# Optimization experiments

Measured on AMD Instinct MI355X. Metric: run time of the kernel, lower is better.

The kernel has to match this reference:

```python
import jax, jax.numpy as jnp
import numpy as np

WS = 8
SHIFT = 4


def _cpb_constants(ws):
    rc = np.arange(-(ws - 1), ws, dtype=np.float32)
    gh, gw = np.meshgrid(rc, rc, indexing='ij')
    table = np.stack([gh, gw], axis=-1)[None]  # (1, 2ws-1, 2ws-1, 2)
    table = table / (ws - 1) * 8.0
    table = np.sign(table) * np.log2(np.abs(table) + 1.0) / np.log2(8.0)
    c = np.arange(ws)
    ch, cw = np.meshgrid(c, c, indexing='ij')
    flat = np.stack([ch.ravel(), cw.ravel()])  # (2, N)
    rel = (flat[:, :, None] - flat[:, None, :]).transpose(1, 2, 0).copy()
    rel[..., 0] += ws - 1
    rel[..., 1] += ws - 1
    rel[..., 0] *= 2 * ws - 1
    rpi = rel.sum(-1)  # (N, N) int
    return table.astype(np.float32), rpi


def _attn_mask(H, W, ws, s):
    # Faithful to source: middle slice is slice(-ws, +s) (empty for H>ws+s)
    img = np.zeros((H, W), np.float32)
    cnt = 0
    for hs in (slice(0, -ws), slice(-ws, s), slice(-s, None)):
        for wsl in (slice(0, -ws), slice(-ws, s), slice(-s, None)):
            img[hs, wsl] = cnt
            cnt += 1
    mw = img.reshape(H // ws, ws, W // ws, ws).transpose(0, 2, 1, 3).reshape(-1, ws * ws)
    am = mw[:, None, :] - mw[:, :, None]
    return np.where(am != 0, -100.0, 0.0).astype(np.float32)


def _dwconv(x, w):
    return jax.lax.conv_general_dilated(
        x, w, (1, 1), 'SAME',
        dimension_numbers=('NCHW', 'OIHW', 'NCHW'),
        feature_group_count=x.shape[1])


def _ln_nchw(x, g, b, eps=8e-8):
    m = x.mean(1, keepdims=True)
    v = jnp.square(x - m).mean(1, keepdims=True)
    return (x - m) / jnp.sqrt(v + eps) * g[None, :, None, None] + b[None, :, None, None]


def setup_inputs() -> dict:
    key = jax.random.key(0)
    ks = jax.random.split(key, 16)
    B, C, H, W = 16, 512, 64, 64
    nh = 16
    hid = 4 * C
    w = lambda k, s: (jax.random.normal(k, s, dtype=jnp.float32) * 0.02)
    return {
        'x': jax.random.normal(ks[0], (B, C, H, W), dtype=jnp.float32),
        'lpu_w': w(ks[1], (C, 1, 3, 3)),
        'qkv_w': w(ks[2], (3 * C, C)),
        'out_w': w(ks[3], (C, C)),
        'cpb_w1': w(ks[4], (512, 2)),
        'cpb_w2': w(ks[5], (nh, 512)),
        'logits_scale': jnp.full((nh, 1, 1), np.log(10.0), dtype=jnp.float32),
        'gamma1': jnp.ones((C,), jnp.float32),
        'beta1': jnp.zeros((C,), jnp.float32),
        'gamma2': jnp.ones((C,), jnp.float32),
        'beta2': jnp.zeros((C,), jnp.float32),
        'pw1_w': w(ks[6], (hid, C)),
        'dw_w': w(ks[7], (hid, 1, 3, 3)),
        'pw2_w': w(ks[8], (C, hid)),
        'sr_scale': jnp.ones((), jnp.float32),
        'sr_bias': jnp.zeros((), jnp.float32),
        'rs1': jnp.ones((C,), jnp.float32),
        'rs2': jnp.ones((C,), jnp.float32),
    }


def reference(x, lpu_w, qkv_w, out_w, cpb_w1, cpb_w2, logits_scale,
              gamma1, beta1, gamma2, beta2, pw1_w, dw_w, pw2_w,
              sr_scale, sr_bias, rs1, rs2):
    B, C, H, W = x.shape
    ws, s = WS, SHIFT
    nh = logits_scale.shape[0]
    hd = C // nh
    N = ws * ws
    table_np, rpi = _cpb_constants(ws)
    table = jnp.asarray(table_np)
    mask = jnp.asarray(_attn_mask(H, W, ws, s))  # (nW, N, N)

    # LPU: x + depthwise conv
    x = x + _dwconv(x, lpu_w)
    x_temp = x

    # flatten to (B, HW, C); faithful roll over dims (1,2) = tokens AND channels
    x = x.reshape(B, C, H * W).transpose(0, 2, 1)
    x = jnp.roll(x, (-s, -s), axis=(1, 2))
    # window partition
    x = x.reshape(B, H // ws, ws, W // ws, ws, C).transpose(0, 1, 3, 2, 4, 5).reshape(-1, N, C)
    Bw = x.shape[0]

    qkv = (x @ qkv_w.T).reshape(Bw, N, 3, nh, hd).transpose(2, 0, 3, 1, 4)
    q, k, v = qkv[0], qkv[1], qkv[2]
    qn = q / jnp.maximum(jnp.linalg.norm(q, axis=-1, keepdims=True), 1e-12)
    kn = k / jnp.maximum(jnp.linalg.norm(k, axis=-1, keepdims=True), 1e-12)
    scale = jnp.exp(jnp.minimum(logits_scale, jnp.log(jnp.float32(100.0))))
    attn = jnp.einsum('bhid,bhjd->bhij', qn, kn) * scale[None]

    # continuous position bias
    tbl = jax.nn.hard_swish(table @ cpb_w1.T) @ cpb_w2.T  # (1, 2ws-1, 2ws-1, nh)
    tbl = tbl.reshape(-1, nh)
    bias = tbl[rpi.reshape(-1)].reshape(N, N, nh).transpose(2, 0, 1)
    bias = 16.0 * jax.nn.sigmoid(bias)
    attn = attn + bias[None]

    nW = mask.shape[0]
    attn = (attn.reshape(Bw // nW, nW, nh, N, N) + mask[None, :, None]).reshape(-1, nh, N, N)
    # faithful: nn.Softmax(1) -> softmax over HEAD axis
    attn = jax.nn.softmax(attn, axis=1)

    o = jnp.einsum('bhij,bhjd->bhid', attn, v).transpose(0, 2, 1, 3).reshape(Bw, N, C)
    o = o @ out_w.T

    o = o.reshape(B, H // ws, ws, W // ws, ws, C)
    o = jnp.roll(o, (s, s), axis=(1, 2))  # faithful: rolls window-grid / row dims
    # faithful buggy un-partition: transpose(1,2) then reshape
    o = o.transpose(0, 2, 1, 3, 4, 5).reshape(B, C, H, W)

    x = rs1[None, :, None, None] * x_temp + _ln_nchw(o, gamma1, beta1)

    h = jnp.einsum('bchw,oc->bohw', x, pw1_w)
    h = h + _dwconv(h, dw_w)
    h = sr_scale * jnp.square(jax.nn.relu(h)) + sr_bias  # StarReLU
    y = jnp.einsum('bchw,oc->bohw', h, pw2_w)
    return rs2[None, :, None, None] * x + _ln_nchw(y, gamma2, beta2)
```

## Files before the change

kernel.cpp:

```cpp
#include <hip/hip_runtime.h>
#include <hip/hip_bf16.h>
#include <stdint.h>


typedef float f32x4 __attribute__((ext_vector_type(4)));
typedef short s16x8 __attribute__((ext_vector_type(8)));

__device__ __forceinline__ float b2f(short u) {
  return __uint_as_float(((unsigned)(unsigned short)u) << 16);
}
__device__ __forceinline__ short f2b(float f) {
  __hip_bfloat16 h = __float2bfloat16(f);
  short s;
  __builtin_memcpy(&s, &h, 2);
  return s;
}
__device__ __forceinline__ void gload16(const void* g, void* l) {
  __builtin_amdgcn_global_load_lds((const unsigned int*)g, (unsigned int*)l, 16, 0, 0);
}

__global__ __launch_bounds__(256) void k_f2b4(const float* __restrict__ s0, short* __restrict__ d0,
                                              const float* __restrict__ s1, short* __restrict__ d1,
                                              const float* __restrict__ s2, short* __restrict__ d2,
                                              const float* __restrict__ s3, short* __restrict__ d3) {
  int b = blockIdx.x;
  const float* s;
  short* d;
  int base;
  if (b < 768) { s = s0; d = d0; base = b * 1024; }
  else if (b < 1024) { s = s1; d = d1; base = (b - 768) * 1024; }
  else if (b < 2048) { s = s2; d = d2; base = (b - 1024) * 1024; }
  else { s = s3; d = d3; base = (b - 2048) * 1024; }
  int i = base + threadIdx.x * 4;
  f32x4 v = *(const f32x4*)&s[i];
  ushort4 o;
  o.x = (unsigned short)f2b(v[0]);
  o.y = (unsigned short)f2b(v[1]);
  o.z = (unsigned short)f2b(v[2]);
  o.w = (unsigned short)f2b(v[3]);
  *(ushort4*)&d[i] = o;
}

__global__ __launch_bounds__(64) void k_cpb(const float* __restrict__ w1,
                                            const float* __restrict__ w2,
                                            float* __restrict__ btab) {
  const int r = blockIdx.x;
  const int lane = threadIdx.x;
  const int ri = r / 15, rj = r % 15;
  float th = (float)(ri - 7) * (8.f / 7.f);
  float tw = (float)(rj - 7) * (8.f / 7.f);
  float gh = copysignf(log2f(fabsf(th) + 1.f) * (1.f / 3.f), th);
  float gw = copysignf(log2f(fabsf(tw) + 1.f) * (1.f / 3.f), tw);
  const int h = lane >> 2, pp = lane & 3;
  float acc = 0.f;
  for (int k = 0; k < 128; ++k) {
    int hh = pp * 128 + k;
    float a = gh * w1[hh * 2] + gw * w1[hh * 2 + 1];
    float r6 = fminf(fmaxf(a + 3.f, 0.f), 6.f);
    float hsw = a * r6 * (1.f / 6.f);
    acc += hsw * w2[h * 512 + hh];
  }
  acc += __shfl_xor(acc, 1);
  acc += __shfl_xor(acc, 2);
  if ((lane & 3) == 0) btab[h * 225 + r] = 16.f / (1.f + __expf(-acc));
}

__global__ __launch_bounds__(256) void k_lpu(const float* __restrict__ x,
                                             const float* __restrict__ lw,
                                             short* __restrict__ xt) {
  __shared__ float img[64 * 68];
  const int bc = blockIdx.x;
  const int c = bc & 511;
  const float* img_g = x + (size_t)bc * 4096;
  short* outp = xt + (size_t)bc * 4096;
  const int tid = threadIdx.x;
#pragma unroll
  for (int t = 0; t < 4; ++t) {
    int idx = t * 256 + tid;
    int h = idx >> 4, w4 = (idx & 15) * 4;
    f32x4 v = *(const f32x4*)&img_g[h * 64 + w4];
    *(f32x4*)&img[h * 68 + w4] = v;
  }
  float wreg[9];
#pragma unroll
  for (int t = 0; t < 9; ++t) wreg[t] = lw[c * 9 + t];
  __syncthreads();
  const int hb = tid >> 4, w0 = (tid & 15) * 4;
#pragma unroll
  for (int g = 0; g < 4; ++g) {
    int h = hb + g * 16;
    float row[3][6];
#pragma unroll
    for (int dr = 0; dr < 3; ++dr) {
      int hh = h - 1 + dr;
      if (hh < 0 || hh > 63) {
#pragma unroll
        for (int j = 0; j < 6; ++j) row[dr][j] = 0.f;
      } else {
        f32x4 m = *(const f32x4*)&img[hh * 68 + w0];
        row[dr][1] = m[0]; row[dr][2] = m[1]; row[dr][3] = m[2]; row[dr][4] = m[3];
        row[dr][0] = (w0 > 0) ? img[hh * 68 + w0 - 1] : 0.f;
        row[dr][5] = (w0 < 60) ? img[hh * 68 + w0 + 4] : 0.f;
      }
    }
    ushort4 o;
    unsigned short op[4];
#pragma unroll
    for (int p = 0; p < 4; ++p) {
      float acc = row[1][p + 1];
#pragma unroll
      for (int dr = 0; dr < 3; ++dr)
#pragma unroll
        for (int dc = 0; dc < 3; ++dc)
          acc += wreg[dr * 3 + dc] * row[dr][p + dc];
      op[p] = (unsigned short)f2b(acc);
    }
    o.x = op[0]; o.y = op[1]; o.z = op[2]; o.w = op[3];
    *(ushort4*)&outp[h * 64 + w0] = o;
  }
}

__global__ __launch_bounds__(256) void k_xpose(const short* __restrict__ xt,
                                               short* __restrict__ xw) {
  __shared__ short tile[64][132];
  const int tid = threadIdx.x;
  const int cq = blockIdx.x & 3;
  const int h = (blockIdx.x >> 2) & 63;
  const int b = blockIdx.x >> 8;
  const int c0 = cq * 128;
  for (int idx = tid; idx < 64 * 128; idx += 256) {
    int ww = idx & 63, cc = idx >> 6;
    int csrc = (c0 + cc + 4) & 511;
    tile[ww][cc] = xt[(((size_t)b * 512 + csrc) * 64 + h) * 64 + ww];
  }
  __syncthreads();
  for (int qd = tid; qd < 64 * 32; qd += 256) {
    int ws_ = qd >> 5, cqq = qd & 31, cc = cqq * 4;
    int t = (h * 64 + ws_ + 4092) & 4095;
    int hd = t >> 6, wd = t & 63;
    int tok = (b * 64 + (hd >> 3) * 8 + (wd >> 3)) * 64 + (hd & 7) * 8 + (wd & 7);
    ushort4 u = *(const ushort4*)&tile[ws_][cc];
    *(ushort4*)&xw[(size_t)tok * 512 + c0 + cc] = u;
  }
}

template <int EPI>
__global__ __launch_bounds__(256) void k_gemm(const short* __restrict__ A,
                                              const short* __restrict__ B,
                                              short* __restrict__ C,
                                              short* __restrict__ o4,
                                              const float* __restrict__ lsc,
                                              int N, int K, int gx) {
  __shared__ short smem[2 * 128 * 64];
  short* As = smem;
  short* Bs = smem + 128 * 64;
  const int nwg = gridDim.x;
  const int orig = blockIdx.x;
  const int wgid = (orig & 7) * (nwg >> 3) + (orig >> 3);
  const int bx = wgid % gx, by = wgid / gx;
  const int tid = threadIdx.x;
  const int lane = tid & 63, wid = tid >> 6;
  const int wm = wid >> 1, wn = wid & 1;
  const int m0 = by * 128, n0 = bx * 128;
  const f32x4 fz = {0.f, 0.f, 0.f, 0.f};
  f32x4 acc[4][4];
#pragma unroll
  for (int m = 0; m < 4; ++m)
#pragma unroll
    for (int n = 0; n < 4; ++n) acc[m][n] = fz;
  const int rst = lane >> 3;
  const int cst = ((lane & 7) ^ rst) * 8;
  const int l15 = lane & 15, l4 = lane >> 4, l7 = lane & 7;
  const short* ap[4];
  const short* bp[4];
#pragma unroll
  for (int i = 0; i < 4; ++i) {
    int r = (i * 4 + wid) * 8 + rst;
    ap[i] = A + (size_t)(m0 + r) * K + cst;
    bp[i] = B + (size_t)(n0 + r) * K + cst;
  }
  for (int k0 = 0; k0 < K; k0 += 64) {
#pragma unroll
    for (int i = 0; i < 4; ++i) {
      int rb = i * 4 + wid;
      gload16(ap[i], As + rb * 512);
      gload16(bp[i], Bs + rb * 512);
      ap[i] += 64;
      bp[i] += 64;
    }
    __syncthreads();
#pragma unroll
    for (int ks = 0; ks < 2; ++ks) {
      s16x8 af[4], bfr[4];
#pragma unroll
      for (int m = 0; m < 4; ++m) {
        int row = wm * 64 + m * 16 + l15;
        af[m] = *(const s16x8*)&As[row * 64 + (((ks * 4 + l4) ^ l7) * 8)];
      }
#pragma unroll
      for (int n = 0; n < 4; ++n) {
        int row = wn * 64 + n * 16 + l15;
        bfr[n] = *(const s16x8*)&Bs[row * 64 + (((ks * 4 + l4) ^ l7) * 8)];
      }
#pragma unroll
      for (int m = 0; m < 4; ++m)
#pragma unroll
        for (int n = 0; n < 4; ++n)
          acc[m][n] = __builtin_amdgcn_mfma_f32_16x16x32_bf16(af[m], bfr[n],
                                                              acc[m][n], 0, 0, 0);
    }
    __syncthreads();
  }
  if (EPI == 2 && n0 < 1024) {
    const int cb = n0 + wn * 64;
    if (cb < 1024) {
      const bool isq = cb < 512;
      float sc0 = 1.f, sc1 = 1.f;
      if (isq) {
        sc0 = __expf(fminf(lsc[cb >> 5], 4.605170185988092f));
        sc1 = __expf(fminf(lsc[(cb >> 5) + 1], 4.605170185988092f));
      }
#pragma unroll
      for (int m = 0; m < 4; ++m)
#pragma unroll
        for (int np = 0; np < 2; ++np)
#pragma unroll
          for (int r = 0; r < 4; ++r) {
            float s0 = acc[m][2 * np][r], s1 = acc[m][2 * np + 1][r];
            float ss = s0 * s0 + s1 * s1;
            ss += __shfl_xor(ss, 1);
            ss += __shfl_xor(ss, 2);
            ss += __shfl_xor(ss, 4);
            ss += __shfl_xor(ss, 8);
            float mul = (np ? sc1 : sc0) / fmaxf(sqrtf(ss), 1e-12f);
            acc[m][2 * np][r] = s0 * mul;
            acc[m][2 * np + 1][r] = s1 * mul;
          }
    }
  }
  short* ct = smem;
  const int colslot = tid & 15;
#pragma unroll
  for (int p = 0; p < 2; ++p) {
    if (p) __syncthreads();
#pragma unroll
    for (int mm = 0; mm < 2; ++mm) {
      int m = p * 2 + mm;
#pragma unroll
      for (int n = 0; n < 4; ++n)
#pragma unroll
        for (int r = 0; r < 4; ++r) {
          int lrow = wm * 32 + mm * 16 + l4 * 4 + r;
          int lc = wn * 64 + n * 16 + l15;
          ct[lrow * 136 + lc] = f2b(acc[m][n][r]);
        }
    }
    __syncthreads();
#pragma unroll
    for (int ps = 0; ps < 4; ++ps) {
      int lr = (tid >> 4) + ps * 16;
      s16x8 v = *(const s16x8*)&ct[lr * 136 + colslot * 8];
      int grow = m0 + (lr >> 5) * 64 + p * 32 + (lr & 31);
      int gcol = n0 + colslot * 8;
      if (EPI != 1) {
        *(s16x8*)&C[(size_t)grow * N + gcol] = v;
      } else {
        int win = grow >> 6, nn = grow & 63;
        int b = win >> 6, whs = (win >> 3) & 7, wws = win & 7;
        int ih = nn >> 3, iw = nn & 7;
        int wh = (whs + 4) & 7, ww = (wws + 4) & 7;
        int cp = ww * 64 + wh * 8 + ih;
        int hp = iw * 8 + (gcol >> 6);
        int wp = gcol & 63;
        *(s16x8*)&o4[(((size_t)b * 512 + cp) * 64 + hp) * 64 + wp] = v;
      }
    }
  }
}

__global__ __launch_bounds__(256) void k_attn(const short* __restrict__ qkv,
                                              const float* __restrict__ btab_g,
                                              short* __restrict__ o_ws) {
  __shared__ float btab[3600];
  __shared__ short vts[2][2048];
  __shared__ short pts[4][1024];
  const int tid = threadIdx.x, lane = tid & 63, wid = tid >> 6;
  const int win = blockIdx.x;
  const int l15 = lane & 15, l4 = lane >> 4;
  const int qrow0 = wid * 16;
  for (int i = tid; i < 3600; i += 256) btab[i] = btab_g[i];
  int baddr[4][4];
#pragma unroll
  for (int n = 0; n < 4; ++n)
#pragma unroll
    for (int r = 0; r < 4; ++r) {
      int i_ = qrow0 + l4 * 4 + r, j_ = n * 16 + l15;
      int dih = (i_ >> 3) - (j_ >> 3) + 7;
      int diw = (i_ & 7) - (j_ & 7) + 7;
      baddr[n][r] = dih * 15 + diw;
    }
  __syncthreads();
  const short* base = qkv + (size_t)win * 64 * 1536;
  const f32x4 fz = {0.f, 0.f, 0.f, 0.f};
  f32x4 sump[4] = {fz, fz, fz, fz};
#pragma unroll 2
  for (int h = 0; h < 16; ++h) {
    s16x8 qf = *(const s16x8*)(base + (size_t)(qrow0 + l15) * 1536 + h * 32 + l4 * 8);
#pragma unroll
    for (int n = 0; n < 4; ++n) {
      s16x8 kf = *(const s16x8*)(base + (size_t)(n * 16 + l15) * 1536 + 512 + h * 32 + l4 * 8);
      f32x4 s = __builtin_amdgcn_mfma_f32_16x16x32_bf16(qf, kf, fz, 0, 0, 0);
#pragma unroll
      for (int r = 0; r < 4; ++r)
        sump[n][r] += __expf(s[r] + btab[h * 225 + baddr[n][r]]);
    }
  }
  f32x4 rden[4];
#pragma unroll
  for (int n = 0; n < 4; ++n)
#pragma unroll
    for (int r = 0; r < 4; ++r) rden[n][r] = 1.f / sump[n][r];
  char* pt = (char*)pts[wid];
  {
    int j = tid & 63, d0 = (tid >> 6) * 8;
    s16x8 vv = *(const s16x8*)(base + (size_t)j * 1536 + 1024 + d0);
#pragma unroll
    for (int jj = 0; jj < 8; ++jj) {
      int d = d0 + jj;
      *(short*)((char*)vts[0] + ((d * 128 + j * 2) ^ ((d & 7) << 4))) = vv[jj];
    }
  }
  __syncthreads();
  for (int h = 0; h < 16; ++h) {
    const char* vcur = (const char*)vts[h & 1];
    if (h < 15) {
      int j = tid & 63, d0 = (tid >> 6) * 8;
      s16x8 vv = *(const s16x8*)(base + (size_t)j * 1536 + 1024 + (h + 1) * 32 + d0);
      char* vnxt = (char*)vts[(h + 1) & 1];
#pragma unroll
      for (int jj = 0; jj < 8; ++jj) {
        int d = d0 + jj;
        *(short*)(vnxt + ((d * 128 + j * 2) ^ ((d & 7) << 4))) = vv[jj];
      }
    }
    s16x8 qf = *(const s16x8*)(base + (size_t)(qrow0 + l15) * 1536 + h * 32 + l4 * 8);
#pragma unroll
    for (int n = 0; n < 4; ++n) {
      s16x8 kf = *(const s16x8*)(base + (size_t)(n * 16 + l15) * 1536 + 512 + h * 32 + l4 * 8);
      f32x4 s = __builtin_amdgcn_mfma_f32_16x16x32_bf16(qf, kf, fz, 0, 0, 0);
#pragma unroll
      for (int r = 0; r < 4; ++r) {
        float pv = __expf(s[r] + btab[h * 225 + baddr[n][r]]) * rden[n][r];
        int i_loc = l4 * 4 + r, j_ = n * 16 + l15;
        *(short*)(pt + ((i_loc * 128 + j_ * 2) ^ ((i_loc & 7) << 4))) = f2b(pv);
      }
    }
    f32x4 oacc[2] = {fz, fz};
#pragma unroll
    for (int kb = 0; kb < 2; ++kb) {
      s16x8 af = *(const s16x8*)(pt + ((l15 * 128 + kb * 64 + l4 * 16) ^ ((l15 & 7) << 4)));
#pragma unroll
      for (int db = 0; db < 2; ++db) {
        int d = db * 16 + l15;
        s16x8 bf = *(const s16x8*)(vcur + ((d * 128 + kb * 64 + l4 * 16) ^ ((d & 7) << 4)));
        oacc[db] = __builtin_amdgcn_mfma_f32_16x16x32_bf16(af, bf, oacc[db], 0, 0, 0);
      }
    }
    short* ob = o_ws + ((size_t)win * 64 + qrow0) * 512 + h * 32;
#pragma unroll
    for (int db = 0; db < 2; ++db)
#pragma unroll
      for (int r = 0; r < 4; ++r)
        ob[(size_t)(l4 * 4 + r) * 512 + db * 16 + l15] = f2b(oacc[db][r]);
    __syncthreads();
  }
}

__global__ __launch_bounds__(256) void k_ln1(const short* __restrict__ o4,
                                             const short* __restrict__ xt,
                                             const float* __restrict__ g1,
                                             const float* __restrict__ b1,
                                             const float* __restrict__ rs1,
                                             short* __restrict__ x2h) {
  __shared__ float reds[4][64], redq[4][64];
  __shared__ float mean_s[64], rstd_s[64];
  __shared__ short tile[128][66];
  const int tid = threadIdx.x;
  const int b = blockIdx.x >> 6, hp = blockIdx.x & 63;
  const int w = tid & 63, part = tid >> 6;
  const short* base = o4 + (size_t)b * 512 * 4096 + hp * 64;
  float s = 0.f, q = 0.f;
  for (int c = part; c < 512; c += 4) {
    float v = b2f(base[(size_t)c * 4096 + w]);
    s += v; q += v * v;
  }
  reds[part][w] = s; redq[part][w] = q;
  __syncthreads();
  if (tid < 64) {
    float S = 0.f, Q = 0.f;
    for (int i = 0; i < 4; ++i) { S += reds[i][tid]; Q += redq[i][tid]; }
    float m = S * (1.f / 512.f);
    float var = Q * (1.f / 512.f) - m * m;
    mean_s[tid] = m;
    rstd_s[tid] = rsqrtf(var + 8e-8f);
  }
  __syncthreads();
  const short* xtb = xt + (size_t)b * 512 * 4096 + hp * 64;
  for (int c0 = 0; c0 < 512; c0 += 128) {
    for (int cc = part; cc < 128; cc += 4) {
      int c = c0 + cc;
      float v = b2f(base[(size_t)c * 4096 + w]);
      float ln = (v - mean_s[w]) * rstd_s[w] * g1[c] + b1[c];
      float xv = rs1[c] * b2f(xtb[(size_t)c * 4096 + w]) + ln;
      tile[cc][w] = f2b(xv);
    }
    __syncthreads();
    short* xh = x2h + ((size_t)blockIdx.x * 64) * 512 + c0;
    for (int qd = tid; qd < 64 * 32; qd += 256) {
      int w_ = qd >> 5, cq = qd & 31, cc = cq * 4;
      ushort4 u;
      u.x = (unsigned short)tile[cc][w_];
      u.y = (unsigned short)tile[cc + 1][w_];
      u.z = (unsigned short)tile[cc + 2][w_];
      u.w = (unsigned short)tile[cc + 3][w_];
      *(ushort4*)&xh[(size_t)w_ * 512 + cc] = u;
    }
    __syncthreads();
  }
}

__global__ __launch_bounds__(256) void k_dwc2(const short* __restrict__ h1,
                                              const float* __restrict__ dw,
                                              const float* __restrict__ srs_p,
                                              const float* __restrict__ srb_p,
                                              short* __restrict__ h2) {
  __shared__ short tile[6 * 64 * 64];
  const int tid = threadIdx.x;
  const int cblk = blockIdx.x & 31;
  const int hq = (blockIdx.x >> 5) & 15;
  const int b = blockIdx.x >> 9;
  const int c0 = cblk * 64;
  const int h0 = hq * 4;
  for (int t = 0; t < 12; ++t) {
    int idx = t * 256 + tid;
    int cg = idx & 7;
    int wl = (idx >> 3) & 63;
    int rl = idx >> 9;
    int hr = h0 - 1 + rl;
    s16x8 v = {0, 0, 0, 0, 0, 0, 0, 0};
    if (hr >= 0 && hr < 64)
      v = *(const s16x8*)&h1[((size_t)b * 4096 + hr * 64 + wl) * 2048 + c0 + cg * 8];
    *(s16x8*)&tile[(rl * 64 + wl) * 64 + (cg ^ (wl & 7)) * 8] = v;
  }
  const int cg = tid & 7;
  const int wq = tid >> 3;
  float wt[9][8];
#pragma unroll
  for (int j = 0; j < 8; ++j) {
    int cch = c0 + cg * 8 + j;
#pragma unroll
    for (int t = 0; t < 9; ++t) wt[t][j] = dw[cch * 9 + t];
  }
  const float srs = *srs_p, srb = *srb_p;
  __syncthreads();
#pragma unroll
  for (int it = 0; it < 8; ++it) {
    int wl = wq + (it & 1) * 32;
    int rl = it >> 1;
    s16x8 ctr = *(const s16x8*)&tile[((rl + 1) * 64 + wl) * 64 + (cg ^ (wl & 7)) * 8];
    float acc[8];
#pragma unroll
    for (int j = 0; j < 8; ++j) acc[j] = b2f(ctr[j]);
#pragma unroll
    for (int dh = -1; dh <= 1; ++dh) {
      int row = rl + 1 + dh;
#pragma unroll
      for (int dwi = -1; dwi <= 1; ++dwi) {
        int wn = wl + dwi;
        if (wn < 0 || wn > 63) continue;
        s16x8 v = *(const s16x8*)&tile[(row * 64 + wn) * 64 + (cg ^ (wn & 7)) * 8];
        const float* wrow = wt[(dh + 1) * 3 + dwi + 1];
#pragma unroll
        for (int j = 0; j < 8; ++j) acc[j] += wrow[j] * b2f(v[j]);
      }
    }
    s16x8 o;
#pragma unroll
    for (int j = 0; j < 8; ++j) {
      float rr = fmaxf(acc[j], 0.f);
      o[j] = f2b(srs * rr * rr + srb);
    }
    *(s16x8*)&h2[((size_t)b * 4096 + (h0 + rl) * 64 + wl) * 2048 + c0 + cg * 8] = o;
  }
}

__global__ __launch_bounds__(256) void k_final(const short* __restrict__ y,
                                               const short* __restrict__ x2h,
                                               const float* __restrict__ g2,
                                               const float* __restrict__ b2p,
                                               const float* __restrict__ rs2,
                                               float* __restrict__ out) {
  __shared__ short yt[64][132];
  __shared__ short xt2[64][132];
  __shared__ float reds[4][64], redq[4][64];
  __shared__ float mean_s[64], rstd_s[64];
  const int tid = threadIdx.x;
  const int b = blockIdx.x >> 6, hh = blockIdx.x & 63;
  const int w = tid & 63, part = tid >> 6;
  const short* yb = y + (size_t)blockIdx.x * 64 * 512;
  const short* xb = x2h + (size_t)blockIdx.x * 64 * 512;
  float s = 0.f, q = 0.f;
  for (int c0 = 0; c0 < 512; c0 += 128) {
    for (int qd = tid; qd < 64 * 32; qd += 256) {
      int w_ = qd >> 5, g = qd & 31;
      *(ushort4*)&yt[w_][g * 4] = *(const ushort4*)&yb[(size_t)w_ * 512 + c0 + g * 4];
    }
    __syncthreads();
    for (int cc = part * 32; cc < part * 32 + 32; ++cc) {
      float v = b2f(yt[w][cc]);
      s += v; q += v * v;
    }
    __syncthreads();
  }
  reds[part][w] = s; redq[part][w] = q;
  __syncthreads();
  if (tid < 64) {
    float S = 0.f, Q = 0.f;
    for (int i = 0; i < 4; ++i) { S += reds[i][tid]; Q += redq[i][tid]; }
    float m = S * (1.f / 512.f);
    float var = Q * (1.f / 512.f) - m * m;
    mean_s[tid] = m;
    rstd_s[tid] = rsqrtf(var + 8e-8f);
  }
  __syncthreads();
  float* ob = out + (size_t)b * 512 * 4096 + hh * 64;
  for (int c0 = 0; c0 < 512; c0 += 128) {
    for (int qd = tid; qd < 64 * 32; qd += 256) {
      int w_ = qd >> 5, g = qd & 31;
      *(ushort4*)&yt[w_][g * 4] = *(const ushort4*)&yb[(size_t)w_ * 512 + c0 + g * 4];
      *(ushort4*)&xt2[w_][g * 4] = *(const ushort4*)&xb[(size_t)w_ * 512 + c0 + g * 4];
    }
    __syncthreads();
    for (int it = 0; it < 32; ++it) {
      int c = c0 + it * 4 + part;
      float yv = b2f(yt[w][c - c0]);
      float lnv = (yv - mean_s[w]) * rstd_s[w] * g2[c] + b2p[c];
      float xv = b2f(xt2[w][c - c0]);
      ob[(size_t)c * 4096 + w] = rs2[c] * xv + lnv;
    }
    __syncthreads();
  }
}

extern "C" void kernel_launch(void* const* d_in, const int* in_sizes, int n_in,
                              void* d_out, int out_size, void* d_ws, size_t ws_size,
                              hipStream_t stream) {
  (void)in_sizes; (void)n_in; (void)out_size; (void)ws_size;
  const float* x      = (const float*)d_in[0];
  const float* lpu_w  = (const float*)d_in[1];
  const float* qkv_w  = (const float*)d_in[2];
  const float* out_w  = (const float*)d_in[3];
  const float* cpb_w1 = (const float*)d_in[4];
  const float* cpb_w2 = (const float*)d_in[5];
  const float* lsc    = (const float*)d_in[6];
  const float* g1     = (const float*)d_in[7];
  const float* b1     = (const float*)d_in[8];
  const float* g2     = (const float*)d_in[9];
  const float* b2v    = (const float*)d_in[10];
  const float* pw1_w  = (const float*)d_in[11];
  const float* dw_w   = (const float*)d_in[12];
  const float* pw2_w  = (const float*)d_in[13];
  const float* srs    = (const float*)d_in[14];
  const float* srb    = (const float*)d_in[15];
  const float* rs1    = (const float*)d_in[16];
  const float* rs2    = (const float*)d_in[17];

  char* ws = (char*)d_ws;
  float* btab   = (float*)(ws + 0);
  short* wbq    = (short*)(ws + 16384);
  short* wbo    = (short*)(ws + 1589248);
  short* wb1    = (short*)(ws + 2113536);
  short* wb2    = (short*)(ws + 4210688);
  short* x_temp = (short*)(ws + 8388608);
  short* xw     = (short*)(ws + 75497472);
  short* qkv    = (short*)(ws + 142606336);
  short* o_ws   = (short*)(ws + 343932928);
  short* o4     = (short*)(ws + 75497472);
  short* x2h    = (short*)(ws + 142606336);
  short* h1     = (short*)(ws + 209715200);
  short* h2     = (short*)(ws + 8388608);
  short* yb     = (short*)(ws + 343932928);

  k_f2b4<<<3072, 256, 0, stream>>>(qkv_w, wbq, out_w, wbo, pw1_w, wb1, pw2_w, wb2);
  k_cpb<<<225, 64, 0, stream>>>(cpb_w1, cpb_w2, btab);
  k_lpu<<<8192, 256, 0, stream>>>(x, lpu_w, x_temp);
  k_xpose<<<4096, 256, 0, stream>>>(x_temp, xw);
  k_gemm<2><<<6144, 256, 0, stream>>>(xw, wbq, qkv, nullptr, lsc, 1536, 512, 12);
  k_attn<<<1024, 256, 0, stream>>>(qkv, btab, o_ws);
  k_gemm<1><<<2048, 256, 0, stream>>>(o_ws, wbo, nullptr, o4, nullptr, 512, 512, 4);
  k_ln1<<<1024, 256, 0, stream>>>(o4, x_temp, g1, b1, rs1, x2h);
  for (int ch = 0; ch < 2; ++ch) {
    const size_t tok0 = (size_t)ch * 8 * 4096;
    k_gemm<0><<<4096, 256, 0, stream>>>(x2h + tok0 * 512, wb1, h1, nullptr, nullptr, 2048, 512, 16);
    k_dwc2<<<4096, 256, 0, stream>>>(h1, dw_w, srs, srb, h2);
    k_gemm<0><<<1024, 256, 0, stream>>>(h2, wb2, yb + tok0 * 512, nullptr, nullptr, 512, 2048, 4);
  }
  k_final<<<1024, 256, 0, stream>>>(yb, x2h, g2, b2v, rs2, (float*)d_out);
}
```

Baseline: 1.169 ms.

## Double-buffer GEMM LDS tiles with 8-wave workgroups and raised MFMA priority

The shared GEMM kernel moves from 4 to 8 waves per 128x128 tile, with each wave computing 64x32. It adds a two-stage LDS ring so the next K-tile's global-to-LDS loads are issued while the current tile is multiplied, and wraps the MFMA section in s_setprio. The epilogue is rewritten for the new wave layout, including the per-head L2 normalisation now done within one wave's 32 columns. The aim is to hide global load latency and raise occupancy, at the cost of twice the LDS per workgroup (64 KB) and fewer accumulators per wave.

```diff
diff --git a/kernel.cpp b/kernel.cpp
--- a/kernel.cpp
+++ b/kernel.cpp
@@ -145,123 +145,121 @@
 }
 
 template <int EPI>
-__global__ __launch_bounds__(256) void k_gemm(const short* __restrict__ A,
+__global__ __launch_bounds__(512) void k_gemm(const short* __restrict__ A,
                                               const short* __restrict__ B,
                                               short* __restrict__ C,
                                               short* __restrict__ o4,
                                               const float* __restrict__ lsc,
                                               int N, int K, int gx) {
-  __shared__ short smem[2 * 128 * 64];
-  short* As = smem;
-  short* Bs = smem + 128 * 64;
+  __shared__ short smem[2 * 16384];
   const int nwg = gridDim.x;
   const int orig = blockIdx.x;
   const int wgid = (orig & 7) * (nwg >> 3) + (orig >> 3);
   const int bx = wgid % gx, by = wgid / gx;
   const int tid = threadIdx.x;
   const int lane = tid & 63, wid = tid >> 6;
-  const int wm = wid >> 1, wn = wid & 1;
+  const int wm = wid >> 2, wn = wid & 3;
   const int m0 = by * 128, n0 = bx * 128;
   const f32x4 fz = {0.f, 0.f, 0.f, 0.f};
-  f32x4 acc[4][4];
-#pragma unroll
-  for (int m = 0; m < 4; ++m)
-#pragma unroll
-    for (int n = 0; n < 4; ++n) acc[m][n] = fz;
+  f32x4 acc[4][2];
+#pragma unroll
+  for (int m = 0; m < 4; ++m) { acc[m][0] = fz; acc[m][1] = fz; }
   const int rst = lane >> 3;
   const int cst = ((lane & 7) ^ rst) * 8;
   const int l15 = lane & 15, l4 = lane >> 4, l7 = lane & 7;
-  const short* ap[4];
-  const short* bp[4];
-#pragma unroll
-  for (int i = 0; i < 4; ++i) {
-    int r = (i * 4 + wid) * 8 + rst;
-    ap[i] = A + (size_t)(m0 + r) * K + cst;
-    bp[i] = B + (size_t)(n0 + r) * K + cst;
-  }
-  for (int k0 = 0; k0 < K; k0 += 64) {
-#pragma unroll
-    for (int i = 0; i < 4; ++i) {
-      int rb = i * 4 + wid;
-      gload16(ap[i], As + rb * 512);
-      gload16(bp[i], Bs + rb * 512);
-      ap[i] += 64;
-      bp[i] += 64;
-    }
-    __syncthreads();
+  const short* ag[2];
+  const short* bg[2];
+#pragma unroll
+  for (int l = 0; l < 2; ++l) {
+    int h8 = wid * 2 + l;
+    ag[l] = A + (size_t)(m0 + h8 * 8 + rst) * K + cst;
+    bg[l] = B + (size_t)(n0 + h8 * 8 + rst) * K + cst;
+  }
+  const int nt = K >> 6;
+  auto STAGE = [&](int b) {
+    short* as = smem + b * 16384;
+    short* bs = as + 8192;
+#pragma unroll
+    for (int l = 0; l < 2; ++l) {
+      int h8 = wid * 2 + l;
+      gload16(ag[l], as + h8 * 512);
+      gload16(bg[l], bs + h8 * 512);
+      ag[l] += 64;
+      bg[l] += 64;
+    }
+  };
+  STAGE(0);
+  __syncthreads();
+  for (int kt = 0; kt < nt; ++kt) {
+    const int cur = kt & 1;
+    if (kt + 1 < nt) STAGE(cur ^ 1);
+    const short* as = smem + cur * 16384;
+    const short* bs = as + 8192;
+    __builtin_amdgcn_s_setprio(1);
 #pragma unroll
     for (int ks = 0; ks < 2; ++ks) {
-      s16x8 af[4], bfr[4];
-#pragma unroll
-      for (int m = 0; m < 4; ++m) {
-        int row = wm * 64 + m * 16 + l15;
-        af[m] = *(const s16x8*)&As[row * 64 + (((ks * 4 + l4) ^ l7) * 8)];
-      }
-#pragma unroll
-      for (int n = 0; n < 4; ++n) {
-        int row = wn * 64 + n * 16 + l15;
-        bfr[n] = *(const s16x8*)&Bs[row * 64 + (((ks * 4 + l4) ^ l7) * 8)];
-      }
+      s16x8 af[4], bfr[2];
 #pragma unroll
       for (int m = 0; m < 4; ++m)
-#pragma unroll
-        for (int n = 0; n < 4; ++n)
+        af[m] = *(const s16x8*)&as[(wm * 64 + m * 16 + l15) * 64 + (((ks * 4 + l4) ^ l7) * 8)];
+#pragma unroll
+      for (int n = 0; n < 2; ++n)
+        bfr[n] = *(const s16x8*)&bs[(wn * 32 + n * 16 + l15) * 64 + (((ks * 4 + l4) ^ l7) * 8)];
+#pragma unroll
+      for (int m = 0; m < 4; ++m)
+#pragma unroll
+        for (int n = 0; n < 2; ++n)
           acc[m][n] = __builtin_amdgcn_mfma_f32_16x16x32_bf16(af[m], bfr[n],
                                                               acc[m][n], 0, 0, 0);
     }
-    __syncthreads();
-  }
-  if (EPI == 2 && n0 < 1024) {
-    const int cb = n0 + wn * 64;
+    __builtin_amdgcn_s_setprio(0);
+    __syncthreads();
+  }
+  if (EPI == 2) {
+    const int cb = n0 + wn * 32;
     if (cb < 1024) {
-      const bool isq = cb < 512;
-      float sc0 = 1.f, sc1 = 1.f;
-      if (isq) {
-        sc0 = __expf(fminf(lsc[cb >> 5], 4.605170185988092f));
-        sc1 = __expf(fminf(lsc[(cb >> 5) + 1], 4.605170185988092f));
-      }
+      float sc = 1.f;
+      if (cb < 512) sc = __expf(fminf(lsc[cb >> 5], 4.605170185988092f));
 #pragma unroll
       for (int m = 0; m < 4; ++m)
 #pragma unroll
-        for (int np = 0; np < 2; ++np)
-#pragma unroll
-          for (int r = 0; r < 4; ++r) {
-            float s0 = acc[m][2 * np][r], s1 = acc[m][2 * np + 1][r];
-            float ss = s0 * s0 + s1 * s1;
-            ss += __shfl_xor(ss, 1);
-            ss += __shfl_xor(ss, 2);
-            ss += __shfl_xor(ss, 4);
-            ss += __shfl_xor(ss, 8);
-            float mul = (np ? sc1 : sc0) / fmaxf(sqrtf(ss), 1e-12f);
-            acc[m][2 * np][r] = s0 * mul;
-            acc[m][2 * np + 1][r] = s1 * mul;
-          }
+        for (int r = 0; r < 4; ++r) {
+          float s0 = acc[m][0][r], s1 = acc[m][1][r];
+          float ss = s0 * s0 + s1 * s1;
+          ss += __shfl_xor(ss, 1);
+          ss += __shfl_xor(ss, 2);
+          ss += __shfl_xor(ss, 4);
+          ss += __shfl_xor(ss, 8);
+          float mul = sc / fmaxf(sqrtf(ss), 1e-12f);
+          acc[m][0][r] = s0 * mul;
+          acc[m][1][r] = s1 * mul;
+        }
     }
   }
   short* ct = smem;
-  const int colslot = tid & 15;
 #pragma unroll
   for (int p = 0; p < 2; ++p) {
     if (p) __syncthreads();
-#pragma unroll
-    for (int mm = 0; mm < 2; ++mm) {
-      int m = p * 2 + mm;
-#pragma unroll
-      for (int n = 0; n < 4; ++n)
-#pragma unroll
-        for (int r = 0; r < 4; ++r) {
-          int lrow = wm * 32 + mm * 16 + l4 * 4 + r;
-          int lc = wn * 64 + n * 16 + l15;
-          ct[lrow * 136 + lc] = f2b(acc[m][n][r]);
-        }
-    }
-    __syncthreads();
-#pragma unroll
-    for (int ps = 0; ps < 4; ++ps) {
-      int lr = (tid >> 4) + ps * 16;
-      s16x8 v = *(const s16x8*)&ct[lr * 136 + colslot * 8];
-      int grow = m0 + (lr >> 5) * 64 + p * 32 + (lr & 31);
-      int gcol = n0 + colslot * 8;
+    if (wm == p) {
+#pragma unroll
+      for (int m = 0; m < 4; ++m)
+#pragma unroll
+        for (int n = 0; n < 2; ++n)
+#pragma unroll
+          for (int r = 0; r < 4; ++r) {
+            int lr = m * 16 + l4 * 4 + r;
+            int lc = wn * 32 + n * 16 + l15;
+            ct[lr * 136 + lc] = f2b(acc[m][n][r]);
+          }
+    }
+    __syncthreads();
+#pragma unroll
+    for (int u = 0; u < 2; ++u) {
+      int unit = u * 512 + tid;
+      int lr = unit >> 4, cs = unit & 15;
+      s16x8 v = *(const s16x8*)&ct[lr * 136 + cs * 8];
+      int grow = m0 + p * 64 + lr;
+      int gcol = n0 + cs * 8;
       if (EPI != 1) {
         *(s16x8*)&C[(size_t)grow * N + gcol] = v;
       } else {
@@ -595,15 +593,15 @@
   k_cpb<<<225, 64, 0, stream>>>(cpb_w1, cpb_w2, btab);
   k_lpu<<<8192, 256, 0, stream>>>(x, lpu_w, x_temp);
   k_xpose<<<4096, 256, 0, stream>>>(x_temp, xw);
-  k_gemm<2><<<6144, 256, 0, stream>>>(xw, wbq, qkv, nullptr, lsc, 1536, 512, 12);
+  k_gemm<2><<<6144, 512, 0, stream>>>(xw, wbq, qkv, nullptr, lsc, 1536, 512, 12);
   k_attn<<<1024, 256, 0, stream>>>(qkv, btab, o_ws);
-  k_gemm<1><<<2048, 256, 0, stream>>>(o_ws, wbo, nullptr, o4, nullptr, 512, 512, 4);
+  k_gemm<1><<<2048, 512, 0, stream>>>(o_ws, wbo, nullptr, o4, nullptr, 512, 512, 4);
   k_ln1<<<1024, 256, 0, stream>>>(o4, x_temp, g1, b1, rs1, x2h);
   for (int ch = 0; ch < 2; ++ch) {
     const size_t tok0 = (size_t)ch * 8 * 4096;
-    k_gemm<0><<<4096, 256, 0, stream>>>(x2h + tok0 * 512, wb1, h1, nullptr, nullptr, 2048, 512, 16);
+    k_gemm<0><<<4096, 512, 0, stream>>>(x2h + tok0 * 512, wb1, h1, nullptr, nullptr, 2048, 512, 16);
     k_dwc2<<<4096, 256, 0, stream>>>(h1, dw_w, srs, srb, h2);
-    k_gemm<0><<<1024, 256, 0, stream>>>(h2, wb2, yb + tok0 * 512, nullptr, nullptr, 512, 2048, 4);
+    k_gemm<0><<<1024, 512, 0, stream>>>(h2, wb2, yb + tok0 * 512, nullptr, nullptr, 512, 2048, 4);
   }
   k_final<<<1024, 256, 0, stream>>>(yb, x2h, g2, b2v, rs2, (float*)d_out);
 }
```

After: 1.107 ms. 1.06x faster.
